# Kernel tuning notes

Measured on AMD Instinct MI355X. Metric: run time of the kernel, lower is better.

## Reference

```python
import jax, jax.numpy as jnp
import numpy as np

N, D_IN, D_KQ, D_V = 4096, 1024, 1024, 1024


def setup_inputs() -> dict:
    key = jax.random.key(0)
    kx, kq, kk, kv = jax.random.split(key, 4)
    return {
        "x": jax.random.normal(kx, (N, D_IN), dtype=jnp.float32),
        "W_query": jax.random.uniform(kq, (D_IN, D_KQ), dtype=jnp.float32),
        "W_key": jax.random.uniform(kk, (D_IN, D_KQ), dtype=jnp.float32),
        "W_value": jax.random.uniform(kv, (D_IN, D_V), dtype=jnp.float32),
        "masked": 1,
    }


def reference(x, W_query, W_key, W_value, masked):
    # x: [N, d_in]; single-head, unbatched attention
    queries = x @ W_query          # [N, d_kq]
    keys = x @ W_key               # [N, d_kq]
    values = x @ W_value           # [N, d_v]
    scores = queries @ keys.T      # [N, N]
    if masked:  # masked is a static Python int
        n = x.shape[0]
        causal = jnp.triu(jnp.ones((n, n), dtype=bool), k=1)
        scores = jnp.where(causal, -jnp.inf, scores)
    scale = 1.0 / jnp.sqrt(jnp.asarray(W_key.shape[1], dtype=scores.dtype))
    attn = jax.nn.softmax(scores * scale, axis=-1)
    return attn @ values           # [N, d_v]
```

## Files before the change

### kernel.cpp

```cpp
#include <hip/hip_runtime.h>
#include <hip/hip_bf16.h>


using bf16 = __hip_bfloat16;
using f32x4 = __attribute__((ext_vector_type(4))) float;
using i32x4 = __attribute__((ext_vector_type(4))) int;
using i8 = signed char;

__device__ __forceinline__ void gload_lds16(const void* g, void* l) {
  __builtin_amdgcn_global_load_lds(
      (const __attribute__((address_space(1))) void*)g,
      (__attribute__((address_space(3))) void*)l, 16, 0, 0);
}

template <int ROWS, int CPR, int NT>
__device__ __forceinline__ void stage_tile8(const i8* __restrict__ g, i8* s,
                                            int ld) {
  const int t = threadIdx.x;
#pragma unroll
  for (int c = 0; c < ROWS * CPR / NT; ++c) {
    const int idx = c * NT + t;
    const int row = idx / CPR;
    const int ch = idx & (CPR - 1);
    const int cg = ch ^ ((row >> 1) & (CPR - 1));
    gload_lds16(g + (size_t)row * ld + cg * 16, s + idx * 16);
  }
}
template <int CPR>
__device__ __forceinline__ i32x4 frag_at8(const i8* s, int row, int ch) {
  return *(const i32x4*)&s[(row * CPR + (ch ^ ((row >> 1) & (CPR - 1)))) * 16];
}

__device__ __forceinline__ i32x4 mfma_i8(i32x4 a, i32x4 b, i32x4 c) {
  return __builtin_amdgcn_mfma_i32_16x16x64_i8(a, b, c, 0, 0, 0);
}

__global__ __launch_bounds__(256, 3) void gemm_qkv_i8(
    const i8* __restrict__ xh, const i8* __restrict__ xl,
    const i8* __restrict__ qTh, const i8* __restrict__ qTl,
    const i8* __restrict__ kTh, const i8* __restrict__ kTl,
    const i8* __restrict__ vTh, const i8* __restrict__ vTl,
    const float* __restrict__ srow, i8* __restrict__ Qh, i8* __restrict__ Ql,
    i8* __restrict__ Kh, i8* __restrict__ Kl, i8* __restrict__ VT) {
  __shared__ __align__(16) i8 sAh[128 * 64], sAl[128 * 64];
  __shared__ __align__(16) i8 sBh[64 * 64], sBl[64 * 64];

  const int bx = blockIdx.x;
  const int which = bx >> 4;
  const int n0 = (bx & 15) * 64;
  const int m0 = blockIdx.y * 128;
  const i8* Bh = which == 0 ? qTh : which == 1 ? kTh : vTh;
  const i8* Bl = which == 0 ? qTl : which == 1 ? kTl : vTl;
  const i8* A_h = xh + (size_t)m0 * 1024;
  const i8* A_l = xl + (size_t)m0 * 1024;
  const i8* B_h = Bh + (size_t)n0 * 1024;
  const i8* B_l = Bl + (size_t)n0 * 1024;

  const int t = threadIdx.x, lane = t & 63, w = t >> 6;
  const int wr = (w >> 1) * 64, wc = (w & 1) * 32;
  const int frow = lane & 15, fc = lane >> 4;

  i32x4 a0[4][2], a1[4][2];
#pragma unroll
  for (int i = 0; i < 4; ++i)
#pragma unroll
    for (int j = 0; j < 2; ++j) {
      a0[i][j] = (i32x4){0, 0, 0, 0};
      a1[i][j] = (i32x4){0, 0, 0, 0};
    }

  for (int kt = 0; kt < 16; ++kt) {
    const int k0 = kt * 64;
    stage_tile8<128, 4, 256>(A_h + k0, sAh, 1024);
    stage_tile8<64, 4, 256>(B_h + k0, sBh, 1024);
    stage_tile8<128, 4, 256>(A_l + k0, sAl, 1024);
    stage_tile8<64, 4, 256>(B_l + k0, sBl, 1024);
    __syncthreads();

    i32x4 ah[4], al[4], bh[2], bl[2];
#pragma unroll
    for (int i = 0; i < 4; ++i) {
      ah[i] = frag_at8<4>(sAh, wr + i * 16 + frow, fc);
      al[i] = frag_at8<4>(sAl, wr + i * 16 + frow, fc);
    }
#pragma unroll
    for (int j = 0; j < 2; ++j) {
      bh[j] = frag_at8<4>(sBh, wc + j * 16 + frow, fc);
      bl[j] = frag_at8<4>(sBl, wc + j * 16 + frow, fc);
    }
#pragma unroll
    for (int i = 0; i < 4; ++i)
#pragma unroll
      for (int j = 0; j < 2; ++j) {
        a0[i][j] = mfma_i8(ah[i], bh[j], a0[i][j]);
        a1[i][j] = mfma_i8(ah[i], bl[j], a1[i][j]);
        a1[i][j] = mfma_i8(al[i], bh[j], a1[i][j]);
      }
    __syncthreads();
  }

  const int er = (lane >> 4) * 4, ec = lane & 15;
  if (which < 2) {
    i8* Ph = which == 0 ? Qh : Kh;
    i8* Pl = which == 0 ? Ql : Kl;
#pragma unroll
    for (int i = 0; i < 4; ++i)
#pragma unroll
      for (int j = 0; j < 2; ++j)
#pragma unroll
        for (int r = 0; r < 4; ++r) {
          const int gm = m0 + wr + i * 16 + er + r;
          const int gn = n0 + wc + j * 16 + ec;
          const float Qf =
              65536.f * (float)a0[i][j][r] + 256.f * (float)a1[i][j][r];
          int q16 = __float2int_rn(Qf * (1.f / 262144.f));
          q16 = min(max(q16, -32511), 32511);
          const int h = (q16 + 128) >> 8;
          const int l = q16 - (h << 8);
          const size_t off = (size_t)gm * 1024 + gn;
          Ph[off] = (i8)h;
          Pl[off] = (i8)l;
        }
  } else {
    const int gm_base = m0 + wr;
#pragma unroll
    for (int i = 0; i < 4; ++i)
#pragma unroll
      for (int j = 0; j < 2; ++j) {
        const int gn = n0 + wc + j * 16 + ec;
        uint pk = 0;
#pragma unroll
        for (int r = 0; r < 4; ++r) {
          const int gm = gm_base + i * 16 + er + r;
          const float Vf =
              (65536.f * (float)a0[i][j][r] + 256.f * (float)a1[i][j][r]) *
                  (1.f / 134217728.f) +
              0.5f * srow[gm];
          int v8 = __float2int_rn(Vf);
          v8 = min(max(v8, -127), 127);
          pk |= (uint)(v8 & 255) << (8 * r);
        }
        *(uint*)(VT + (size_t)gn * 4096 + gm_base + i * 16 + er) = pk;
      }
  }
}

__global__ __launch_bounds__(256, 3) void gemm_s_i8(
    const i8* __restrict__ Qh, const i8* __restrict__ Ql,
    const i8* __restrict__ Kh, const i8* __restrict__ Kl,
    const float* __restrict__ srow, const float* __restrict__ qsum,
    const float* __restrict__ ksum, float* __restrict__ S) {
  const int cb = blockIdx.x, rb = blockIdx.y;
  if (cb > 2 * rb + 1) return;
  const int n0 = cb * 64, m0 = rb * 128;
  __shared__ __align__(16) i8 sAh[128 * 64], sAl[128 * 64];
  __shared__ __align__(16) i8 sBh[64 * 64], sBl[64 * 64];

  const i8* A_h = Qh + (size_t)m0 * 1024;
  const i8* A_l = Ql + (size_t)m0 * 1024;
  const i8* B_h = Kh + (size_t)n0 * 1024;
  const i8* B_l = Kl + (size_t)n0 * 1024;

  const int t = threadIdx.x, lane = t & 63, w = t >> 6;
  const int wr = (w >> 1) * 64, wc = (w & 1) * 32;
  const int frow = lane & 15, fc = lane >> 4;

  i32x4 a0[4][2], a1[4][2];
#pragma unroll
  for (int i = 0; i < 4; ++i)
#pragma unroll
    for (int j = 0; j < 2; ++j) {
      a0[i][j] = (i32x4){0, 0, 0, 0};
      a1[i][j] = (i32x4){0, 0, 0, 0};
    }

  for (int kt = 0; kt < 16; ++kt) {
    const int k0 = kt * 64;
    stage_tile8<128, 4, 256>(A_h + k0, sAh, 1024);
    stage_tile8<64, 4, 256>(B_h + k0, sBh, 1024);
    stage_tile8<128, 4, 256>(A_l + k0, sAl, 1024);
    stage_tile8<64, 4, 256>(B_l + k0, sBl, 1024);
    __syncthreads();

    i32x4 ah[4], al[4], bh[2], bl[2];
#pragma unroll
    for (int i = 0; i < 4; ++i) {
      ah[i] = frag_at8<4>(sAh, wr + i * 16 + frow, fc);
      al[i] = frag_at8<4>(sAl, wr + i * 16 + frow, fc);
    }
#pragma unroll
    for (int j = 0; j < 2; ++j) {
      bh[j] = frag_at8<4>(sBh, wc + j * 16 + frow, fc);
      bl[j] = frag_at8<4>(sBl, wc + j * 16 + frow, fc);
    }
#pragma unroll
    for (int i = 0; i < 4; ++i)
#pragma unroll
      for (int j = 0; j < 2; ++j) {
        a0[i][j] = mfma_i8(ah[i], bh[j], a0[i][j]);
        a1[i][j] = mfma_i8(ah[i], bl[j], a1[i][j]);
        a1[i][j] = mfma_i8(al[i], bh[j], a1[i][j]);
      }
    __syncthreads();
  }

  const int er = (lane >> 4) * 4, ec = lane & 15;
  float sn[2], kn[2];
#pragma unroll
  for (int j = 0; j < 2; ++j) {
    const int gn = n0 + wc + j * 16 + ec;
    sn[j] = srow[gn];
    kn[j] = ksum[gn];
  }
#pragma unroll
  for (int i = 0; i < 4; ++i)
#pragma unroll
    for (int r = 0; r < 4; ++r) {
      const int gm = m0 + wr + i * 16 + er + r;
      const float sm = srow[gm], qm = qsum[gm];
#pragma unroll
      for (int j = 0; j < 2; ++j) {
        const int gn = n0 + wc + j * 16 + ec;
        const float Sf =
            65536.f * (float)a0[i][j][r] + 256.f * (float)a1[i][j][r];
        const float logit = Sf * (1.f / 8388608.f) +
                            0.015625f * (sn[j] * qm + sm * kn[j]) +
                            8.f * sm * sn[j];
        S[(size_t)gm * 4096 + gn] = logit;
      }
    }
}

__global__ __launch_bounds__(256, 4) void gemm_pv_i8(
    const i8* __restrict__ P, const i8* __restrict__ VT,
    const float* __restrict__ inv_s, float* __restrict__ O) {
  __shared__ __align__(16) i8 sP[128 * 64];
  __shared__ __align__(16) i8 sV[64 * 64];

  const int bxr = blockIdx.x;
  const int rb = (bxr & 1) ? (31 - (bxr >> 1)) : (bxr >> 1);
  const int m0 = rb * 128;
  const int n0 = blockIdx.y * 64;
  const int ktiles = 2 * (rb + 1);

  const i8* A0 = P + (size_t)m0 * 4096;
  const i8* B0 = VT + (size_t)n0 * 4096;

  const int t = threadIdx.x, lane = t & 63, w = t >> 6;
  const int wr = (w >> 1) * 64, wc = (w & 1) * 32;
  const int frow = lane & 15, fc = lane >> 4;

  i32x4 a0[4][2];
#pragma unroll
  for (int i = 0; i < 4; ++i)
#pragma unroll
    for (int j = 0; j < 2; ++j) a0[i][j] = (i32x4){0, 0, 0, 0};

  for (int kt = 0; kt < ktiles; ++kt) {
    const int k0 = kt * 64;
    stage_tile8<128, 4, 256>(A0 + k0, sP, 4096);
    stage_tile8<64, 4, 256>(B0 + k0, sV, 4096);
    __syncthreads();

    i32x4 pa[4], b[2];
#pragma unroll
    for (int i = 0; i < 4; ++i) pa[i] = frag_at8<4>(sP, wr + i * 16 + frow, fc);
#pragma unroll
    for (int j = 0; j < 2; ++j) b[j] = frag_at8<4>(sV, wc + j * 16 + frow, fc);
#pragma unroll
    for (int i = 0; i < 4; ++i)
#pragma unroll
      for (int j = 0; j < 2; ++j) a0[i][j] = mfma_i8(pa[i], b[j], a0[i][j]);
    __syncthreads();
  }

  const int er = (lane >> 4) * 4, ec = lane & 15;
#pragma unroll
  for (int i = 0; i < 4; ++i)
#pragma unroll
    for (int j = 0; j < 2; ++j)
#pragma unroll
      for (int r = 0; r < 4; ++r) {
        const int gm = m0 + wr + i * 16 + er + r;
        const int gn = n0 + wc + j * 16 + ec;
        O[(size_t)gm * 1024 + gn] =
            (float)a0[i][j][r] * inv_s[gm] * (1.f / 127.f);
      }
}

__global__ __launch_bounds__(256) void softmax_kernel(
    const float* __restrict__ S, i8* __restrict__ P,
    float* __restrict__ inv_s, int N) {
  const int wid = threadIdx.x >> 6;
  const int r0 = blockIdx.x * 2 + (wid >> 1);
  const int row = (wid & 1) ? (N - 1 - r0) : r0;
  const int lane = threadIdx.x & 63;
  const float* s = S + (size_t)row * N;
  i8* p = P + (size_t)row * N;
  const int len = row + 1;
  const int nv4 = len >> 2;
  const float4* s4 = (const float4*)s;

  float m = -3.4e38f;
  for (int j = lane; j < nv4; j += 64) {
    const float4 v = s4[j];
    m = fmaxf(m, fmaxf(fmaxf(v.x, v.y), fmaxf(v.z, v.w)));
  }
  for (int j = (nv4 << 2) + lane; j < len; j += 64) m = fmaxf(m, s[j]);
#pragma unroll
  for (int off = 32; off > 0; off >>= 1) m = fmaxf(m, __shfl_xor(m, off, 64));

  float sum = 0.f;
  for (int j = lane; j < nv4; j += 64) {
    const float4 v = s4[j];
    const float e0 = __expf(v.x - m), e1 = __expf(v.y - m);
    const float e2 = __expf(v.z - m), e3 = __expf(v.w - m);
    sum += (e0 + e1) + (e2 + e3);
    uint pk = (uint)__float2int_rn(e0 * 127.f);
    pk |= (uint)__float2int_rn(e1 * 127.f) << 8;
    pk |= (uint)__float2int_rn(e2 * 127.f) << 16;
    pk |= (uint)__float2int_rn(e3 * 127.f) << 24;
    *(uint*)(p + 4 * j) = pk;
  }
  for (int j = (nv4 << 2) + lane; j < len; j += 64) {
    const float e = __expf(s[j] - m);
    sum += e;
    p[j] = (i8)__float2int_rn(e * 127.f);
  }
#pragma unroll
  for (int off = 32; off > 0; off >>= 1) sum += __shfl_xor(sum, off, 64);

  const int bound = ((row >> 7) + 1) << 7;
  for (int j = len + lane; j < bound; j += 64) p[j] = (i8)0;
  if (lane == 0) inv_s[row] = 1.f / sum;
}

__global__ void split_x_i8(const float4* __restrict__ x, uint* __restrict__ h,
                           uint* __restrict__ l, int n4) {
  const int i = blockIdx.x * blockDim.x + threadIdx.x;
  if (i >= n4) return;
  const float4 v = x[i];
  const float f[4] = {v.x, v.y, v.z, v.w};
  uint hp = 0, lp = 0;
#pragma unroll
  for (int k = 0; k < 4; ++k) {
    int q = __float2int_rn(f[k] * 4096.f);
    q = min(max(q, -32511), 32511);
    const int hh = (q + 128) >> 8;
    const int ll = q - (hh << 8);
    hp |= (uint)(hh & 255) << (8 * k);
    lp |= (uint)(ll & 255) << (8 * k);
  }
  h[i] = hp;
  l[i] = lp;
}

__global__ void split_transpose_w_i8(
    const float* __restrict__ W0, const float* __restrict__ W1,
    const float* __restrict__ W2, i8* __restrict__ T0h, i8* __restrict__ T0l,
    i8* __restrict__ T1h, i8* __restrict__ T1l, i8* __restrict__ T2h,
    i8* __restrict__ T2l, int R, int C) {
  const int z = blockIdx.z;
  const float* W = z == 0 ? W0 : z == 1 ? W1 : W2;
  i8* Th = z == 0 ? T0h : z == 1 ? T1h : T2h;
  i8* Tl = z == 0 ? T0l : z == 1 ? T1l : T2l;
  __shared__ float tile[32][33];
  const int c0 = blockIdx.x * 32, r0 = blockIdx.y * 32;
  const int tx = threadIdx.x, ty = threadIdx.y;
  for (int rr = ty; rr < 32; rr += 8)
    tile[rr][tx] = W[(size_t)(r0 + rr) * C + c0 + tx];
  __syncthreads();
  for (int cc = ty; cc < 32; cc += 8) {
    const float v = tile[tx][cc] - 0.5f;
    int w16 = __float2int_rn(v * 32768.f);
    w16 = min(max(w16, -32511), 32511);
    const int h = (w16 + 128) >> 8;
    const int l = w16 - (h << 8);
    const size_t off = (size_t)(c0 + cc) * R + r0 + tx;
    Th[off] = (i8)h;
    Tl[off] = (i8)l;
  }
}

__global__ __launch_bounds__(256) void wrow_kernel(const float* __restrict__ Wq,
                                                   const float* __restrict__ Wk,
                                                   float* __restrict__ wqrow,
                                                   float* __restrict__ wkrow) {
  const int k = blockIdx.x * 4 + (threadIdx.x >> 6);
  const int lane = threadIdx.x & 63;
  const float* W = blockIdx.y == 0 ? Wq : Wk;
  float* out = blockIdx.y == 0 ? wqrow : wkrow;
  const float* row = W + (size_t)k * 1024;
  float s = 0.f;
  for (int c = lane; c < 1024; c += 64) s += row[c];
#pragma unroll
  for (int off = 32; off > 0; off >>= 1) s += __shfl_xor(s, off, 64);
  if (lane == 0) out[k] = s - 512.f;
}

__global__ __launch_bounds__(256) void rowstats_kernel(
    const float* __restrict__ x, const float* __restrict__ wqrow,
    const float* __restrict__ wkrow, float* __restrict__ srow,
    float* __restrict__ qsum, float* __restrict__ ksum) {
  const int i = blockIdx.x * 4 + (threadIdx.x >> 6);
  const int lane = threadIdx.x & 63;
  const float* row = x + (size_t)i * 1024;
  float ss = 0.f, sq = 0.f, sk = 0.f;
  for (int c = lane; c < 1024; c += 64) {
    const float v = row[c];
    ss += v;
    sq += v * wqrow[c];
    sk += v * wkrow[c];
  }
#pragma unroll
  for (int off = 32; off > 0; off >>= 1) {
    ss += __shfl_xor(ss, off, 64);
    sq += __shfl_xor(sq, off, 64);
    sk += __shfl_xor(sk, off, 64);
  }
  if (lane == 0) {
    srow[i] = ss;
    qsum[i] = sq;
    ksum[i] = sk;
  }
}

extern "C" void kernel_launch(void* const* d_in, const int* in_sizes, int n_in,
                              void* d_out, int out_size, void* d_ws,
                              size_t ws_size, hipStream_t stream) {
  (void)in_sizes; (void)n_in; (void)out_size; (void)ws_size;
  const float* x = (const float*)d_in[0];
  const float* Wq = (const float*)d_in[1];
  const float* Wk = (const float*)d_in[2];
  const float* Wv = (const float*)d_in[3];

  const int N = 4096, D = 1024;

  char* p = (char*)d_ws;
  auto alloc = [&](size_t bytes) {
    char* r = p;
    p += (bytes + 255) & ~(size_t)255;
    return r;
  };
  i8* xh = (i8*)alloc((size_t)N * D);
  i8* xl = (i8*)alloc((size_t)N * D);
  i8* WqTh = (i8*)alloc((size_t)D * D);
  i8* WqTl = (i8*)alloc((size_t)D * D);
  i8* WkTh = (i8*)alloc((size_t)D * D);
  i8* WkTl = (i8*)alloc((size_t)D * D);
  i8* WvTh = (i8*)alloc((size_t)D * D);
  i8* WvTl = (i8*)alloc((size_t)D * D);
  i8* Qh = (i8*)alloc((size_t)N * D);
  i8* Ql = (i8*)alloc((size_t)N * D);
  i8* Kh = (i8*)alloc((size_t)N * D);
  i8* Kl = (i8*)alloc((size_t)N * D);
  i8* VT = (i8*)alloc((size_t)D * N);
  float* S = (float*)alloc((size_t)N * N * 4);
  i8* P = (i8*)alloc((size_t)N * N);
  float* inv_s = (float*)alloc((size_t)N * 4);
  float* srow = (float*)alloc((size_t)N * 4);
  float* qsum = (float*)alloc((size_t)N * 4);
  float* ksum = (float*)alloc((size_t)N * 4);
  float* wqrow = (float*)alloc((size_t)D * 4);
  float* wkrow = (float*)alloc((size_t)D * 4);

  split_x_i8<<<N * D / 4 / 256, 256, 0, stream>>>((const float4*)x, (uint*)xh,
                                                  (uint*)xl, N * D / 4);
  split_transpose_w_i8<<<dim3(32, 32, 3), dim3(32, 8), 0, stream>>>(
      Wq, Wk, Wv, WqTh, WqTl, WkTh, WkTl, WvTh, WvTl, D, D);
  wrow_kernel<<<dim3(D / 4, 2), 256, 0, stream>>>(Wq, Wk, wqrow, wkrow);
  rowstats_kernel<<<N / 4, 256, 0, stream>>>(x, wqrow, wkrow, srow, qsum, ksum);

  gemm_qkv_i8<<<dim3(48, 32), 256, 0, stream>>>(xh, xl, WqTh, WqTl, WkTh, WkTl,
                                                WvTh, WvTl, srow, Qh, Ql, Kh,
                                                Kl, VT);

  gemm_s_i8<<<dim3(64, 32), 256, 0, stream>>>(Qh, Ql, Kh, Kl, srow, qsum, ksum,
                                              S);

  softmax_kernel<<<N / 4, 256, 0, stream>>>(S, P, inv_s, N);

  gemm_pv_i8<<<dim3(32, 16), 256, 0, stream>>>(P, VT, inv_s, (float*)d_out);
}
```

Before: 234.5 us.

## Double-buffer LDS tiles in int8 GEMM kernels to overlap loads with MFMA

All three int8 GEMM kernels (QKV projection, score, and PV) now keep two LDS buffers per tile. The next k-tile is issued with async global-to-LDS loads right after the barrier, and the MFMAs then run on the current buffer, which removes one barrier per iteration. This is meant to hide global load latency behind compute. It doubles LDS use per block, which may cut occupancy below the launch_bounds targets. With global_load_lds, correctness also depends on the barrier's implicit vmcnt wait covering the async copy into the buffer being read.

```diff
diff --git a/kernel.cpp b/kernel.cpp
--- a/kernel.cpp
+++ b/kernel.cpp
@@ -42,8 +42,8 @@
     const i8* __restrict__ vTh, const i8* __restrict__ vTl,
     const float* __restrict__ srow, i8* __restrict__ Qh, i8* __restrict__ Ql,
     i8* __restrict__ Kh, i8* __restrict__ Kl, i8* __restrict__ VT) {
-  __shared__ __align__(16) i8 sAh[128 * 64], sAl[128 * 64];
-  __shared__ __align__(16) i8 sBh[64 * 64], sBl[64 * 64];
+  __shared__ __align__(16) i8 sAh[2][128 * 64], sAl[2][128 * 64];
+  __shared__ __align__(16) i8 sBh[2][64 * 64], sBl[2][64 * 64];
 
   const int bx = blockIdx.x;
   const int which = bx >> 4;
@@ -69,24 +69,29 @@
       a1[i][j] = (i32x4){0, 0, 0, 0};
     }
 
+  auto stage_all = [&](int k0, int s) {
+    stage_tile8<128, 4, 256>(A_h + k0, sAh[s], 1024);
+    stage_tile8<64, 4, 256>(B_h + k0, sBh[s], 1024);
+    stage_tile8<128, 4, 256>(A_l + k0, sAl[s], 1024);
+    stage_tile8<64, 4, 256>(B_l + k0, sBl[s], 1024);
+  };
+
+  stage_all(0, 0);
+  int cur = 0;
   for (int kt = 0; kt < 16; ++kt) {
-    const int k0 = kt * 64;
-    stage_tile8<128, 4, 256>(A_h + k0, sAh, 1024);
-    stage_tile8<64, 4, 256>(B_h + k0, sBh, 1024);
-    stage_tile8<128, 4, 256>(A_l + k0, sAl, 1024);
-    stage_tile8<64, 4, 256>(B_l + k0, sBl, 1024);
     __syncthreads();
+    if (kt < 15) stage_all((kt + 1) * 64, cur ^ 1);
 
     i32x4 ah[4], al[4], bh[2], bl[2];
 #pragma unroll
     for (int i = 0; i < 4; ++i) {
-      ah[i] = frag_at8<4>(sAh, wr + i * 16 + frow, fc);
-      al[i] = frag_at8<4>(sAl, wr + i * 16 + frow, fc);
+      ah[i] = frag_at8<4>(sAh[cur], wr + i * 16 + frow, fc);
+      al[i] = frag_at8<4>(sAl[cur], wr + i * 16 + frow, fc);
     }
 #pragma unroll
     for (int j = 0; j < 2; ++j) {
-      bh[j] = frag_at8<4>(sBh, wc + j * 16 + frow, fc);
-      bl[j] = frag_at8<4>(sBl, wc + j * 16 + frow, fc);
+      bh[j] = frag_at8<4>(sBh[cur], wc + j * 16 + frow, fc);
+      bl[j] = frag_at8<4>(sBl[cur], wc + j * 16 + frow, fc);
     }
 #pragma unroll
     for (int i = 0; i < 4; ++i)
@@ -96,7 +101,7 @@
         a1[i][j] = mfma_i8(ah[i], bl[j], a1[i][j]);
         a1[i][j] = mfma_i8(al[i], bh[j], a1[i][j]);
       }
-    __syncthreads();
+    cur ^= 1;
   }
 
   const int er = (lane >> 4) * 4, ec = lane & 15;
@@ -153,8 +158,8 @@
   const int cb = blockIdx.x, rb = blockIdx.y;
   if (cb > 2 * rb + 1) return;
   const int n0 = cb * 64, m0 = rb * 128;
-  __shared__ __align__(16) i8 sAh[128 * 64], sAl[128 * 64];
-  __shared__ __align__(16) i8 sBh[64 * 64], sBl[64 * 64];
+  __shared__ __align__(16) i8 sAh[2][128 * 64], sAl[2][128 * 64];
+  __shared__ __align__(16) i8 sBh[2][64 * 64], sBl[2][64 * 64];
 
   const i8* A_h = Qh + (size_t)m0 * 1024;
   const i8* A_l = Ql + (size_t)m0 * 1024;
@@ -174,24 +179,29 @@
       a1[i][j] = (i32x4){0, 0, 0, 0};
     }
 
+  auto stage_all = [&](int k0, int s) {
+    stage_tile8<128, 4, 256>(A_h + k0, sAh[s], 1024);
+    stage_tile8<64, 4, 256>(B_h + k0, sBh[s], 1024);
+    stage_tile8<128, 4, 256>(A_l + k0, sAl[s], 1024);
+    stage_tile8<64, 4, 256>(B_l + k0, sBl[s], 1024);
+  };
+
+  stage_all(0, 0);
+  int cur = 0;
   for (int kt = 0; kt < 16; ++kt) {
-    const int k0 = kt * 64;
-    stage_tile8<128, 4, 256>(A_h + k0, sAh, 1024);
-    stage_tile8<64, 4, 256>(B_h + k0, sBh, 1024);
-    stage_tile8<128, 4, 256>(A_l + k0, sAl, 1024);
-    stage_tile8<64, 4, 256>(B_l + k0, sBl, 1024);
     __syncthreads();
+    if (kt < 15) stage_all((kt + 1) * 64, cur ^ 1);
 
     i32x4 ah[4], al[4], bh[2], bl[2];
 #pragma unroll
     for (int i = 0; i < 4; ++i) {
-      ah[i] = frag_at8<4>(sAh, wr + i * 16 + frow, fc);
-      al[i] = frag_at8<4>(sAl, wr + i * 16 + frow, fc);
+      ah[i] = frag_at8<4>(sAh[cur], wr + i * 16 + frow, fc);
+      al[i] = frag_at8<4>(sAl[cur], wr + i * 16 + frow, fc);
     }
 #pragma unroll
     for (int j = 0; j < 2; ++j) {
-      bh[j] = frag_at8<4>(sBh, wc + j * 16 + frow, fc);
-      bl[j] = frag_at8<4>(sBl, wc + j * 16 + frow, fc);
+      bh[j] = frag_at8<4>(sBh[cur], wc + j * 16 + frow, fc);
+      bl[j] = frag_at8<4>(sBl[cur], wc + j * 16 + frow, fc);
     }
 #pragma unroll
     for (int i = 0; i < 4; ++i)
@@ -201,7 +211,7 @@
         a1[i][j] = mfma_i8(ah[i], bl[j], a1[i][j]);
         a1[i][j] = mfma_i8(al[i], bh[j], a1[i][j]);
       }
-    __syncthreads();
+    cur ^= 1;
   }
 
   const int er = (lane >> 4) * 4, ec = lane & 15;
@@ -234,8 +244,8 @@
 __global__ __launch_bounds__(256, 4) void gemm_pv_i8(
     const i8* __restrict__ P, const i8* __restrict__ VT,
     const float* __restrict__ inv_s, float* __restrict__ O) {
-  __shared__ __align__(16) i8 sP[128 * 64];
-  __shared__ __align__(16) i8 sV[64 * 64];
+  __shared__ __align__(16) i8 sP[2][128 * 64];
+  __shared__ __align__(16) i8 sV[2][64 * 64];
 
   const int bxr = blockIdx.x;
   const int rb = (bxr & 1) ? (31 - (bxr >> 1)) : (bxr >> 1);
@@ -256,22 +266,29 @@
 #pragma unroll
     for (int j = 0; j < 2; ++j) a0[i][j] = (i32x4){0, 0, 0, 0};
 
+  auto stage_all = [&](int k0, int s) {
+    stage_tile8<128, 4, 256>(A0 + k0, sP[s], 4096);
+    stage_tile8<64, 4, 256>(B0 + k0, sV[s], 4096);
+  };
+
+  stage_all(0, 0);
+  int cur = 0;
   for (int kt = 0; kt < ktiles; ++kt) {
-    const int k0 = kt * 64;
-    stage_tile8<128, 4, 256>(A0 + k0, sP, 4096);
-    stage_tile8<64, 4, 256>(B0 + k0, sV, 4096);
     __syncthreads();
+    if (kt + 1 < ktiles) stage_all((kt + 1) * 64, cur ^ 1);
 
     i32x4 pa[4], b[2];
 #pragma unroll
-    for (int i = 0; i < 4; ++i) pa[i] = frag_at8<4>(sP, wr + i * 16 + frow, fc);
-#pragma unroll
-    for (int j = 0; j < 2; ++j) b[j] = frag_at8<4>(sV, wc + j * 16 + frow, fc);
-#pragma unroll
     for (int i = 0; i < 4; ++i)
+      pa[i] = frag_at8<4>(sP[cur], wr + i * 16 + frow, fc);
+#pragma unroll
+    for (int j = 0; j < 2; ++j)
+      b[j] = frag_at8<4>(sV[cur], wc + j * 16 + frow, fc);
+#pragma unroll
+    for (int i = 0; i < 4; ++i)
 #pragma unroll
       for (int j = 0; j < 2; ++j) a0[i][j] = mfma_i8(pa[i], b[j], a0[i][j]);
-    __syncthreads();
+    cur ^= 1;
   }
 
   const int er = (lane >> 4) * 4, ec = lane & 15;
```

New measurement: 236.8 us. Within noise of the previous version (+1.0%).

## Triple-buffer LDS staging with async prefetch two tiles ahead in int8 GEMMs

Applied to the files above, without the earlier changes.

Converts the QKV, score and PV int8 GEMM kernels from single-buffered LDS staging to a three-stage ring. Global-to-LDS loads for tile k+2 are issued while tile k is being computed. Partial vmcnt waits plus a single barrier per iteration replace the two __syncthreads, and MFMA sections are raised in priority with s_setprio. This is meant to hide global load latency behind MFMA work. In exchange, LDS use triples and launch bounds for two kernels drop from 3 to 2 blocks per CU, which reduces occupancy.

```diff
diff --git a/kernel.cpp b/kernel.cpp
--- a/kernel.cpp
+++ b/kernel.cpp
@@ -35,15 +35,30 @@
   return __builtin_amdgcn_mfma_i32_16x16x64_i8(a, b, c, 0, 0, 0);
 }
 
-__global__ __launch_bounds__(256, 3) void gemm_qkv_i8(
+__device__ __forceinline__ void wait_vm6() {
+  asm volatile("s_waitcnt vmcnt(6)" ::: "memory");
+}
+__device__ __forceinline__ void wait_vm3() {
+  asm volatile("s_waitcnt vmcnt(3)" ::: "memory");
+}
+__device__ __forceinline__ void wait_vm0() {
+  asm volatile("s_waitcnt vmcnt(0)" ::: "memory");
+}
+__device__ __forceinline__ void barrier_pipe() {
+  __builtin_amdgcn_s_barrier();
+  __builtin_amdgcn_sched_barrier(0);
+}
+
+__global__ __launch_bounds__(256, 2) void gemm_qkv_i8(
     const i8* __restrict__ xh, const i8* __restrict__ xl,
     const i8* __restrict__ qTh, const i8* __restrict__ qTl,
     const i8* __restrict__ kTh, const i8* __restrict__ kTl,
     const i8* __restrict__ vTh, const i8* __restrict__ vTl,
     const float* __restrict__ srow, i8* __restrict__ Qh, i8* __restrict__ Ql,
     i8* __restrict__ Kh, i8* __restrict__ Kl, i8* __restrict__ VT) {
-  __shared__ __align__(16) i8 sAh[128 * 64], sAl[128 * 64];
-  __shared__ __align__(16) i8 sBh[64 * 64], sBl[64 * 64];
+  constexpr int TA = 128 * 64, TB = 64 * 64;
+  __shared__ __align__(16) i8 sAh[3 * TA], sAl[3 * TA];
+  __shared__ __align__(16) i8 sBh[3 * TB], sBl[3 * TB];
 
   const int bx = blockIdx.x;
   const int which = bx >> 4;
@@ -69,25 +84,45 @@
       a1[i][j] = (i32x4){0, 0, 0, 0};
     }
 
+  auto stage_all = [&](int kt, int b) {
+    const int k0 = kt * 64;
+    stage_tile8<128, 4, 256>(A_h + k0, sAh + b * TA, 1024);
+    stage_tile8<64, 4, 256>(B_h + k0, sBh + b * TB, 1024);
+    stage_tile8<128, 4, 256>(A_l + k0, sAl + b * TA, 1024);
+    stage_tile8<64, 4, 256>(B_l + k0, sBl + b * TB, 1024);
+  };
+
+  stage_all(0, 0);
+  stage_all(1, 1);
+  int rd = 0;
   for (int kt = 0; kt < 16; ++kt) {
-    const int k0 = kt * 64;
-    stage_tile8<128, 4, 256>(A_h + k0, sAh, 1024);
-    stage_tile8<64, 4, 256>(B_h + k0, sBh, 1024);
-    stage_tile8<128, 4, 256>(A_l + k0, sAl, 1024);
-    stage_tile8<64, 4, 256>(B_l + k0, sBl, 1024);
-    __syncthreads();
-
+    if (kt < 15)
+      wait_vm6();
+    else
+      wait_vm0();
+    barrier_pipe();
+
+    const i8* pAh = sAh + rd * TA;
+    const i8* pAl = sAl + rd * TA;
+    const i8* pBh = sBh + rd * TB;
+    const i8* pBl = sBl + rd * TB;
     i32x4 ah[4], al[4], bh[2], bl[2];
 #pragma unroll
     for (int i = 0; i < 4; ++i) {
-      ah[i] = frag_at8<4>(sAh, wr + i * 16 + frow, fc);
-      al[i] = frag_at8<4>(sAl, wr + i * 16 + frow, fc);
+      ah[i] = frag_at8<4>(pAh, wr + i * 16 + frow, fc);
+      al[i] = frag_at8<4>(pAl, wr + i * 16 + frow, fc);
     }
 #pragma unroll
     for (int j = 0; j < 2; ++j) {
-      bh[j] = frag_at8<4>(sBh, wc + j * 16 + frow, fc);
-      bl[j] = frag_at8<4>(sBl, wc + j * 16 + frow, fc);
-    }
+      bh[j] = frag_at8<4>(pBh, wc + j * 16 + frow, fc);
+      bl[j] = frag_at8<4>(pBl, wc + j * 16 + frow, fc);
+    }
+
+    int st = rd + 2;
+    if (st >= 3) st -= 3;
+    if (kt + 2 < 16) stage_all(kt + 2, st);
+
+    __builtin_amdgcn_s_setprio(1);
 #pragma unroll
     for (int i = 0; i < 4; ++i)
 #pragma unroll
@@ -96,7 +131,8 @@
         a1[i][j] = mfma_i8(ah[i], bl[j], a1[i][j]);
         a1[i][j] = mfma_i8(al[i], bh[j], a1[i][j]);
       }
-    __syncthreads();
+    __builtin_amdgcn_s_setprio(0);
+    rd = (rd == 2) ? 0 : rd + 1;
   }
 
   const int er = (lane >> 4) * 4, ec = lane & 15;
@@ -145,7 +181,7 @@
   }
 }
 
-__global__ __launch_bounds__(256, 3) void gemm_s_i8(
+__global__ __launch_bounds__(256, 2) void gemm_s_i8(
     const i8* __restrict__ Qh, const i8* __restrict__ Ql,
     const i8* __restrict__ Kh, const i8* __restrict__ Kl,
     const float* __restrict__ srow, const float* __restrict__ qsum,
@@ -153,8 +189,9 @@
   const int cb = blockIdx.x, rb = blockIdx.y;
   if (cb > 2 * rb + 1) return;
   const int n0 = cb * 64, m0 = rb * 128;
-  __shared__ __align__(16) i8 sAh[128 * 64], sAl[128 * 64];
-  __shared__ __align__(16) i8 sBh[64 * 64], sBl[64 * 64];
+  constexpr int TA = 128 * 64, TB = 64 * 64;
+  __shared__ __align__(16) i8 sAh[3 * TA], sAl[3 * TA];
+  __shared__ __align__(16) i8 sBh[3 * TB], sBl[3 * TB];
 
   const i8* A_h = Qh + (size_t)m0 * 1024;
   const i8* A_l = Ql + (size_t)m0 * 1024;
@@ -174,25 +211,45 @@
       a1[i][j] = (i32x4){0, 0, 0, 0};
     }
 
+  auto stage_all = [&](int kt, int b) {
+    const int k0 = kt * 64;
+    stage_tile8<128, 4, 256>(A_h + k0, sAh + b * TA, 1024);
+    stage_tile8<64, 4, 256>(B_h + k0, sBh + b * TB, 1024);
+    stage_tile8<128, 4, 256>(A_l + k0, sAl + b * TA, 1024);
+    stage_tile8<64, 4, 256>(B_l + k0, sBl + b * TB, 1024);
+  };
+
+  stage_all(0, 0);
+  stage_all(1, 1);
+  int rd = 0;
   for (int kt = 0; kt < 16; ++kt) {
-    const int k0 = kt * 64;
-    stage_tile8<128, 4, 256>(A_h + k0, sAh, 1024);
-    stage_tile8<64, 4, 256>(B_h + k0, sBh, 1024);
-    stage_tile8<128, 4, 256>(A_l + k0, sAl, 1024);
-    stage_tile8<64, 4, 256>(B_l + k0, sBl, 1024);
-    __syncthreads();
-
+    if (kt < 15)
+      wait_vm6();
+    else
+      wait_vm0();
+    barrier_pipe();
+
+    const i8* pAh = sAh + rd * TA;
+    const i8* pAl = sAl + rd * TA;
+    const i8* pBh = sBh + rd * TB;
+    const i8* pBl = sBl + rd * TB;
     i32x4 ah[4], al[4], bh[2], bl[2];
 #pragma unroll
     for (int i = 0; i < 4; ++i) {
-      ah[i] = frag_at8<4>(sAh, wr + i * 16 + frow, fc);
-      al[i] = frag_at8<4>(sAl, wr + i * 16 + frow, fc);
+      ah[i] = frag_at8<4>(pAh, wr + i * 16 + frow, fc);
+      al[i] = frag_at8<4>(pAl, wr + i * 16 + frow, fc);
     }
 #pragma unroll
     for (int j = 0; j < 2; ++j) {
-      bh[j] = frag_at8<4>(sBh, wc + j * 16 + frow, fc);
-      bl[j] = frag_at8<4>(sBl, wc + j * 16 + frow, fc);
-    }
+      bh[j] = frag_at8<4>(pBh, wc + j * 16 + frow, fc);
+      bl[j] = frag_at8<4>(pBl, wc + j * 16 + frow, fc);
+    }
+
+    int st = rd + 2;
+    if (st >= 3) st -= 3;
+    if (kt + 2 < 16) stage_all(kt + 2, st);
+
+    __builtin_amdgcn_s_setprio(1);
 #pragma unroll
     for (int i = 0; i < 4; ++i)
 #pragma unroll
@@ -201,7 +258,8 @@
         a1[i][j] = mfma_i8(ah[i], bl[j], a1[i][j]);
         a1[i][j] = mfma_i8(al[i], bh[j], a1[i][j]);
       }
-    __syncthreads();
+    __builtin_amdgcn_s_setprio(0);
+    rd = (rd == 2) ? 0 : rd + 1;
   }
 
   const int er = (lane >> 4) * 4, ec = lane & 15;
@@ -234,8 +292,9 @@
 __global__ __launch_bounds__(256, 4) void gemm_pv_i8(
     const i8* __restrict__ P, const i8* __restrict__ VT,
     const float* __restrict__ inv_s, float* __restrict__ O) {
-  __shared__ __align__(16) i8 sP[128 * 64];
-  __shared__ __align__(16) i8 sV[64 * 64];
+  constexpr int TA = 128 * 64, TB = 64 * 64;
+  __shared__ __align__(16) i8 sP[3 * TA];
+  __shared__ __align__(16) i8 sV[3 * TB];
 
   const int bxr = blockIdx.x;
   const int rb = (bxr & 1) ? (31 - (bxr >> 1)) : (bxr >> 1);
@@ -256,22 +315,41 @@
 #pragma unroll
     for (int j = 0; j < 2; ++j) a0[i][j] = (i32x4){0, 0, 0, 0};
 
+  auto stage_all = [&](int kt, int b) {
+    const int k0 = kt * 64;
+    stage_tile8<128, 4, 256>(A0 + k0, sP + b * TA, 4096);
+    stage_tile8<64, 4, 256>(B0 + k0, sV + b * TB, 4096);
+  };
+
+  stage_all(0, 0);
+  stage_all(1, 1);
+  int rd = 0;
   for (int kt = 0; kt < ktiles; ++kt) {
-    const int k0 = kt * 64;
-    stage_tile8<128, 4, 256>(A0 + k0, sP, 4096);
-    stage_tile8<64, 4, 256>(B0 + k0, sV, 4096);
-    __syncthreads();
-
+    if (kt + 1 < ktiles)
+      wait_vm3();
+    else
+      wait_vm0();
+    barrier_pipe();
+
+    const i8* pP = sP + rd * TA;
+    const i8* pV = sV + rd * TB;
     i32x4 pa[4], b[2];
 #pragma unroll
-    for (int i = 0; i < 4; ++i) pa[i] = frag_at8<4>(sP, wr + i * 16 + frow, fc);
-#pragma unroll
-    for (int j = 0; j < 2; ++j) b[j] = frag_at8<4>(sV, wc + j * 16 + frow, fc);
+    for (int i = 0; i < 4; ++i) pa[i] = frag_at8<4>(pP, wr + i * 16 + frow, fc);
+#pragma unroll
+    for (int j = 0; j < 2; ++j) b[j] = frag_at8<4>(pV, wc + j * 16 + frow, fc);
+
+    int st = rd + 2;
+    if (st >= 3) st -= 3;
+    if (kt + 2 < ktiles) stage_all(kt + 2, st);
+
+    __builtin_amdgcn_s_setprio(1);
 #pragma unroll
     for (int i = 0; i < 4; ++i)
 #pragma unroll
       for (int j = 0; j < 2; ++j) a0[i][j] = mfma_i8(pa[i], b[j], a0[i][j]);
-    __syncthreads();
+    __builtin_amdgcn_s_setprio(0);
+    rd = (rd == 2) ? 0 : rd + 1;
   }
 
   const int er = (lane >> 4) * 4, ec = lane & 15;
```

Result: no change. 234.4 us (-0.1%).
